# Optimization experiments

Hardware: AMD Instinct MI355X
Metric: run time of the kernel (lower is better)

Reference implementation:

```python
import jax, jax.numpy as jnp
import numpy as np

N_NODES = 150000
D = 64
N_EDGES = 2000000  # bidirectional: 2 * num_train_edges


def setup_inputs() -> dict:
    key = jax.random.key(0)
    k1, k2, k3, k4, k5 = jax.random.split(key, 5)
    nodes_emb = jax.random.normal(k1, (N_NODES, D), dtype=jnp.float32)
    src = jax.random.randint(k2, (N_EDGES,), 0, N_NODES, dtype=jnp.int64 if jax.config.jax_enable_x64 else jnp.int32).astype(jnp.int32)
    dst = jax.random.randint(k3, (N_EDGES,), 0, N_NODES, dtype=jnp.int32)
    W1 = jax.random.normal(k4, (2 * D, D), dtype=jnp.float32) * (1.0 / np.sqrt(2 * D))
    b1 = jnp.zeros((D,), dtype=jnp.float32)
    W2 = jax.random.normal(k5, (D, 1), dtype=jnp.float32) * (1.0 / np.sqrt(D))
    b2 = jnp.zeros((1,), dtype=jnp.float32)
    return {"nodes_emb": nodes_emb, "src": src, "dst": dst,
            "W1": W1, "b1": b1, "W2": W2, "b2": b2}


def reference(nodes_emb, src, dst, W1, b1, W2, b2):
    # Gather per-edge endpoint embeddings and concat: [E, 2D]
    emb_src = nodes_emb[src]          # [E, D]
    emb_dst = nodes_emb[dst]          # [E, D]
    edge_emb = jnp.concatenate([emb_src, emb_dst], axis=1)  # [E, 2D]
    # 2-layer MLP edge scorer: Linear(2D->D) -> ReLU -> Linear(D->1)
    h = jax.nn.relu(edge_emb @ W1 + b1)  # [E, D]
    edge_logits = h @ W2 + b2            # [E, 1]
    return edge_logits
```

## Files before the change

kernel.cpp:

```cpp
#include <hip/hip_runtime.h>
#include <math.h>

typedef __attribute__((ext_vector_type(8))) short bf16x8;
typedef __attribute__((ext_vector_type(4))) float f32x4;
typedef __attribute__((ext_vector_type(2))) unsigned int u32x2;
typedef __attribute__((ext_vector_type(4))) unsigned int u32x4;
typedef unsigned long long u64;

#define LDSTR 136
#define TPW 8
#define NREP 128
#define NBKT 64

static __device__ __forceinline__ unsigned int pack2bf(float x, float y) {
  unsigned int ux = __builtin_bit_cast(unsigned int, x);
  ux += 0x7fffu + ((ux >> 16) & 1u);
  unsigned int uy = __builtin_bit_cast(unsigned int, y);
  uy += 0x7fffu + ((uy >> 16) & 1u);
  return (ux >> 16) | (uy & 0xffff0000u);
}
static __device__ __forceinline__ unsigned short f2bf_s(float x) {
  unsigned int ux = __builtin_bit_cast(unsigned int, x);
  ux += 0x7fffu + ((ux >> 16) & 1u);
  return (unsigned short)(ux >> 16);
}
static __device__ __forceinline__ bf16x8 make_afrag(float4 lo, float4 hi) {
  u32x4 p;
  p[0] = pack2bf(lo.x, lo.y);
  p[1] = pack2bf(lo.z, lo.w);
  p[2] = pack2bf(hi.x, hi.y);
  p[3] = pack2bf(hi.z, hi.w);
  return __builtin_bit_cast(bf16x8, p);
}

static __device__ __forceinline__ unsigned int q8(float v, float inv) {
  return (unsigned int)((int)rintf(v * inv) + 128);
}

static __device__ __forceinline__ float dot8i(u32x2 P, u32x2 Q, float sp, float sq,
                                              const float* w2v) {
  const float t_ = -128.f * (sp + sq);
  float acc = 0.f;
  #pragma unroll
  for (int k2 = 0; k2 < 2; ++k2) {
    const unsigned int pd = P[k2], qd = Q[k2];
    #pragma unroll
    for (int b = 0; b < 4; ++b) {
      float pf = (float)((pd >> (8 * b)) & 0xffu);
      float qf = (float)((qd >> (8 * b)) & 0xffu);
      float h = __builtin_fmaf(pf, sp, __builtin_fmaf(qf, sq, t_));
      h = fmaxf(h, 0.f);
      acc = __builtin_fmaf(h, w2v[k2 * 4 + b], acc);
    }
  }
  return acc;
}

__global__ __launch_bounds__(256) void node_proj(
    const float* __restrict__ emb, const float* __restrict__ W1,
    const float* __restrict__ b1,
    unsigned int* __restrict__ P8, unsigned int* __restrict__ Q8,
    float* __restrict__ SP, float* __restrict__ SQ, int N, int ntiles)
{
  __shared__ unsigned short ls_w1t[64 * LDSTR];
  const int tid  = threadIdx.x;
  const int wave = tid >> 6;
  const int lane = tid & 63;
  const int l15  = lane & 15;
  const int quad = lane >> 4;

  for (int i = tid; i < 64 * 128; i += 256) {
    int k = i >> 6, n = i & 63;
    ls_w1t[n * LDSTR + k] = f2bf_s(W1[i]);
  }
  __syncthreads();

  float b1q[4];
  #pragma unroll
  for (int tn = 0; tn < 4; ++tn) b1q[tn] = b1[tn * 16 + l15];

  bf16x8 bfragP[4][2], bfragQ[4][2];
  #pragma unroll
  for (int tn = 0; tn < 4; ++tn)
    #pragma unroll
    for (int s = 0; s < 2; ++s) {
      bfragP[tn][s] = *(const bf16x8*)&ls_w1t[(tn * 16 + l15) * LDSTR + s * 32 + quad * 8];
      bfragQ[tn][s] = *(const bf16x8*)&ls_w1t[(tn * 16 + l15) * LDSTR + 64 + s * 32 + quad * 8];
    }

  for (int tile = blockIdx.x * 4 + wave; tile < ntiles; tile += gridDim.x * 4) {
    const int base = tile * 16;

    bf16x8 afr0, afr1;
    {
      int node = base + l15;
      node = (node < N) ? node : N - 1;
      const float* rp = emb + (long long)node * 64 + quad * 8;
      afr0 = make_afrag(*(const float4*)(rp),      *(const float4*)(rp + 4));
      afr1 = make_afrag(*(const float4*)(rp + 32), *(const float4*)(rp + 36));
    }

    f32x4 aP[4], aQ[4];
    #pragma unroll
    for (int tn = 0; tn < 4; ++tn) { aP[tn] = (f32x4){0,0,0,0}; aQ[tn] = (f32x4){0,0,0,0}; }
    #pragma unroll
    for (int tn = 0; tn < 4; ++tn) {
      aP[tn] = __builtin_amdgcn_mfma_f32_16x16x32_bf16(afr0, bfragP[tn][0], aP[tn], 0, 0, 0);
      aQ[tn] = __builtin_amdgcn_mfma_f32_16x16x32_bf16(afr0, bfragQ[tn][0], aQ[tn], 0, 0, 0);
      aP[tn] = __builtin_amdgcn_mfma_f32_16x16x32_bf16(afr1, bfragP[tn][1], aP[tn], 0, 0, 0);
      aQ[tn] = __builtin_amdgcn_mfma_f32_16x16x32_bf16(afr1, bfragQ[tn][1], aQ[tn], 0, 0, 0);
    }

    #pragma unroll
    for (int r = 0; r < 4; ++r) {
      const int m = base + quad * 4 + r;
      float vp0 = aP[0][r], vp1 = aP[1][r], vp2 = aP[2][r], vp3 = aP[3][r];
      float vq0 = aQ[0][r] + b1q[0], vq1 = aQ[1][r] + b1q[1];
      float vq2 = aQ[2][r] + b1q[2], vq3 = aQ[3][r] + b1q[3];

      float mp = fmaxf(fmaxf(fabsf(vp0), fabsf(vp1)), fmaxf(fabsf(vp2), fabsf(vp3)));
      float mq = fmaxf(fmaxf(fabsf(vq0), fabsf(vq1)), fmaxf(fabsf(vq2), fabsf(vq3)));
      mp = fmaxf(mp, __shfl_xor(mp, 1)); mq = fmaxf(mq, __shfl_xor(mq, 1));
      mp = fmaxf(mp, __shfl_xor(mp, 2)); mq = fmaxf(mq, __shfl_xor(mq, 2));
      mp = fmaxf(mp, __shfl_xor(mp, 4)); mq = fmaxf(mq, __shfl_xor(mq, 4));
      mp = fmaxf(mp, __shfl_xor(mp, 8)); mq = fmaxf(mq, __shfl_xor(mq, 8));

      const float invP = (mp > 0.f) ? 127.f / mp : 0.f;
      const float invQ = (mq > 0.f) ? 127.f / mq : 0.f;

      if (m < N) {
        unsigned int pw = q8(vp0, invP) | (q8(vp1, invP) << 8) |
                          (q8(vp2, invP) << 16) | (q8(vp3, invP) << 24);
        unsigned int qw = q8(vq0, invQ) | (q8(vq1, invQ) << 8) |
                          (q8(vq2, invQ) << 16) | (q8(vq3, invQ) << 24);
        P8[(long long)m * 16 + l15] = pw;
        Q8[(long long)m * 16 + l15] = qw;
        if (l15 == 0) {
          SP[m] = mp * (1.f / 127.f);
          SQ[m] = mq * (1.f / 127.f);
        }
      }
    }
  }
}

__global__ __launch_bounds__(256) void bucketize(
    const int* __restrict__ src, const int* __restrict__ dst,
    const float* __restrict__ SP, const float* __restrict__ SQ,
    u32x2* __restrict__ seg, unsigned short* __restrict__ posrec,
    unsigned int* __restrict__ cntT, int E, int ndiv, int cap)
{
  __shared__ unsigned int curs[NBKT];
  const int r = blockIdx.x;
  const int per = (E + NREP - 1) / NREP;
  const int lo = r * per;
  const int hi = (lo + per < E) ? lo + per : E;
  for (int i = threadIdx.x; i < NBKT; i += 256) curs[i] = 0;
  __syncthreads();

  for (int e0 = lo + threadIdx.x; e0 < hi; e0 += 1024) {
    const int e1 = e0 + 256, e2 = e0 + 512, e3 = e0 + 768;
    const int e1c = (e1 < hi) ? e1 : hi - 1;
    const int e2c = (e2 < hi) ? e2 : hi - 1;
    const int e3c = (e3 < hi) ? e3 : hi - 1;
    const int s0 = src[e0],  d0 = dst[e0];
    const int s1 = src[e1c], d1 = dst[e1c];
    const int s2 = src[e2c], d2 = dst[e2c];
    const int s3 = src[e3c], d3 = dst[e3c];
    const float sp0 = SP[s0], sq0 = SQ[d0];
    const float sp1 = SP[s1], sq1 = SQ[d1];
    const float sp2 = SP[s2], sq2 = SQ[d2];
    const float sp3 = SP[s3], sq3 = SQ[d3];

#define BK_PROC(EE, SS, DD, SPV, SQV)                                         \
    {                                                                         \
      const int bi = (SS) / ndiv, bj = (DD) / ndiv;                           \
      const int bkt = bi * 8 + bj;                                            \
      const unsigned int pos = atomicAdd(&curs[bkt], 1u);                     \
      unsigned short pr = 0xFFFFu;                                            \
      if (pos < (unsigned)cap) {                                              \
        u32x2 ev;                                                             \
        ev[0] = (unsigned)((SS) - bi * ndiv) |                                \
                ((unsigned)((DD) - bj * ndiv) << 15);                         \
        ev[1] = ((unsigned)f2bf_s(SPV) << 16) | (unsigned)f2bf_s(SQV);        \
        seg[((size_t)(r * NBKT + bkt)) * cap + pos] = ev;                     \
        pr = (unsigned short)(((unsigned)bkt << 9) | pos);                    \
      }                                                                       \
      posrec[EE] = pr;                                                        \
    }

    BK_PROC(e0, s0, d0, sp0, sq0);
    if (e1 < hi) BK_PROC(e1, s1, d1, sp1, sq1);
    if (e2 < hi) BK_PROC(e2, s2, d2, sp2, sq2);
    if (e3 < hi) BK_PROC(e3, s3, d3, sp3, sq3);
#undef BK_PROC
  }
  __syncthreads();
  for (int bkt = threadIdx.x; bkt < NBKT; bkt += 256) {
    unsigned int c = curs[bkt];
    cntT[bkt * NREP + r] = (c < (unsigned)cap) ? c : (unsigned)cap;
  }
}

__global__ __launch_bounds__(256) void edge_score_seg(
    const unsigned int* __restrict__ P8, const unsigned int* __restrict__ Q8,
    const u32x2* __restrict__ seg, const unsigned int* __restrict__ cntT,
    const float* __restrict__ W2, const float* __restrict__ b2,
    float* __restrict__ tmp, int cap, int ndiv)
{
  const int tid  = threadIdx.x;
  const int lane = tid & 63;
  const int sv   = lane & 7;
  const int g    = lane >> 3;
  const int k    = blockIdx.x & 7;
  const int tblk = blockIdx.x >> 3;
  const int wgid = tblk * 4 + (tid >> 6);
  const int r    = wgid >> 3;
  const int sub  = wgid & 7;

  float w2v[8];
  #pragma unroll
  for (int j = 0; j < 8; ++j) {
    const int pos = sv * 8 + j;
    const int ch  = (pos & 3) * 16 + (pos >> 2);
    w2v[j] = W2[ch];
  }
  const float b2v = b2[0];
  const int sd = sv * 2;
  const int sbase = k * ndiv;

  int cnts[8];
  #pragma unroll
  for (int j = 0; j < 8; ++j) cnts[j] = (int)cntT[(k * 8 + j) * NREP + r];

  #pragma unroll 1
  for (int j = 0; j < 8; ++j) {
    const int b = k * 8 + j;
    const int dbase = j * ndiv;
    const int cnt = cnts[j];
    const int chunk = (cnt + 7) >> 3;
    const int lo = sub * chunk;
    const int hi = (cnt < lo + chunk) ? cnt : lo + chunk;
    if (lo >= hi) continue;
    const u32x2* sgp = seg + (size_t)(r * NBKT + b) * cap;
    float* tp = tmp + (size_t)(r * NBKT + b) * cap;

    #pragma unroll 2
    for (int m = lo + g; m < hi; m += 8) {
      const u32x2 v = sgp[m];
      const int s_ = sbase + (int)(v[0] & 0x7FFFu);
      const int d_ = dbase + (int)(v[0] >> 15);
      const float sp = __builtin_bit_cast(float, v[1] & 0xffff0000u);
      const float sq = __builtin_bit_cast(float, v[1] << 16);

      const u32x2 pv = *(const u32x2*)(P8 + s_ * 16 + sd);
      const u32x2 qv = *(const u32x2*)(Q8 + d_ * 16 + sd);

      float acc = dot8i(pv, qv, sp, sq, w2v);
      acc += __shfl_xor(acc, 1);
      acc += __shfl_xor(acc, 2);
      acc += __shfl_xor(acc, 4);
      if (sv == 0) tp[m] = acc + b2v;
    }
  }
}

__global__ __launch_bounds__(256) void unscatter(
    const unsigned short* __restrict__ posrec, const float* __restrict__ tmp,
    float* __restrict__ out,
    const int* __restrict__ src, const int* __restrict__ dst,
    const unsigned int* __restrict__ P8, const unsigned int* __restrict__ Q8,
    const float* __restrict__ SP, const float* __restrict__ SQ,
    const float* __restrict__ W2, const float* __restrict__ b2,
    int E, int per, int cap)
{
  const int r   = blockIdx.x >> 3;
  const int sub = blockIdx.x & 7;
  const int lo_r = r * per;
  int lenr = E - lo_r;
  if (lenr <= 0) return;
  if (lenr > per) lenr = per;
  const int chunk = (lenr + 7) >> 3;
  const int lo = lo_r + sub * chunk;
  int hi = lo + chunk;
  const int end_r = lo_r + lenr;
  if (hi > end_r) hi = end_r;
  const float* tb = tmp + (size_t)r * NBKT * cap;

  for (int e = lo + threadIdx.x; e < hi; e += 256) {
    const unsigned int pr = posrec[e];
    if (pr != 0xFFFFu) {
      out[e] = tb[(pr >> 9) * cap + (pr & 511u)];
    } else {
      const int s_ = src[e], d_ = dst[e];
      const float sp = SP[s_], sq = SQ[d_];
      const float t_ = -128.f * (sp + sq);
      float acc = 0.f;
      for (int w = 0; w < 16; ++w) {
        const unsigned int pd = P8[(size_t)s_ * 16 + w];
        const unsigned int qd = Q8[(size_t)d_ * 16 + w];
        for (int bb = 0; bb < 4; ++bb) {
          const int pos = w * 4 + bb;
          const int ch  = (pos & 3) * 16 + (pos >> 2);
          float pf = (float)((pd >> (8 * bb)) & 0xffu);
          float qf = (float)((qd >> (8 * bb)) & 0xffu);
          float h = __builtin_fmaf(pf, sp, __builtin_fmaf(qf, sq, t_));
          h = fmaxf(h, 0.f);
          acc = __builtin_fmaf(h, W2[ch], acc);
        }
      }
      out[e] = acc + b2[0];
    }
  }
}

__global__ __launch_bounds__(256) void edge_score(
    const unsigned int* __restrict__ P8, const unsigned int* __restrict__ Q8,
    const float* __restrict__ SP, const float* __restrict__ SQ,
    const int* __restrict__ src, const int* __restrict__ dst,
    const float* __restrict__ W2, const float* __restrict__ b2,
    float* __restrict__ out, int E)
{
  const int tid  = blockIdx.x * 256 + threadIdx.x;
  const int lane = threadIdx.x & 63;
  const int s    = lane & 7;
  const int g    = lane >> 3;
  const int wid  = tid >> 6;
  const int step = gridDim.x * 4 * 32;

  float w2v[8];
  #pragma unroll
  for (int j = 0; j < 8; ++j) {
    const int pos = s * 8 + j;
    const int ch  = (pos & 3) * 16 + (pos >> 2);
    w2v[j] = W2[ch];
  }
  const float b2v = b2[0];
  const int sd = s * 2;

  int e0 = wid * 32;
  if (e0 >= E) return;

  int iA, iB, iC, iD, jA, jB, jC, jD;
  {
    const int eA = e0 + g,      eAc = (eA < E) ? eA : E - 1;
    const int eB = e0 + 8 + g,  eBc = (eB < E) ? eB : E - 1;
    const int eC = e0 + 16 + g, eCc = (eC < E) ? eC : E - 1;
    const int eD = e0 + 24 + g, eDc = (eD < E) ? eD : E - 1;
    iA = src[eAc]; jA = dst[eAc];
    iB = src[eBc]; jB = dst[eBc];
    iC = src[eCc]; jC = dst[eCc];
    iD = src[eDc]; jD = dst[eDc];
  }
  float spA = SP[iA], sqA = SQ[jA];
  float spB = SP[iB], sqB = SQ[jB];
  float spC = SP[iC], sqC = SQ[jC];
  float spD = SP[iD], sqD = SQ[jD];

  while (true) {
    const u32x2 pA = *(const u32x2*)(P8 + iA * 16 + sd);
    const u32x2 qA = *(const u32x2*)(Q8 + jA * 16 + sd);
    const u32x2 pB = *(const u32x2*)(P8 + iB * 16 + sd);
    const u32x2 qB = *(const u32x2*)(Q8 + jB * 16 + sd);
    const u32x2 pC = *(const u32x2*)(P8 + iC * 16 + sd);
    const u32x2 qC = *(const u32x2*)(Q8 + jC * 16 + sd);
    const u32x2 pD = *(const u32x2*)(P8 + iD * 16 + sd);
    const u32x2 qD = *(const u32x2*)(Q8 + jD * 16 + sd);

    const int en = e0 + step;
    const bool more = (en < E);
    int nA = iA, nB = iB, nC = iC, nD = iD;
    int mA = jA, mB = jB, mC = jC, mD = jD;
    if (more) {
      const int fA = en + g,      fAc = (fA < E) ? fA : E - 1;
      const int fB = en + 8 + g,  fBc = (fB < E) ? fB : E - 1;
      const int fC = en + 16 + g, fCc = (fC < E) ? fC : E - 1;
      const int fD = en + 24 + g, fDc = (fD < E) ? fD : E - 1;
      nA = src[fAc]; mA = dst[fAc];
      nB = src[fBc]; mB = dst[fBc];
      nC = src[fCc]; mC = dst[fCc];
      nD = src[fDc]; mD = dst[fDc];
    }

    float accA = dot8i(pA, qA, spA, sqA, w2v);
    float accB = dot8i(pB, qB, spB, sqB, w2v);
    float accC = dot8i(pC, qC, spC, sqC, w2v);
    float accD = dot8i(pD, qD, spD, sqD, w2v);

    accA += __shfl_xor(accA, 1); accB += __shfl_xor(accB, 1);
    accC += __shfl_xor(accC, 1); accD += __shfl_xor(accD, 1);
    accA += __shfl_xor(accA, 2); accB += __shfl_xor(accB, 2);
    accC += __shfl_xor(accC, 2); accD += __shfl_xor(accD, 2);
    accA += __shfl_xor(accA, 4); accB += __shfl_xor(accB, 4);
    accC += __shfl_xor(accC, 4); accD += __shfl_xor(accD, 4);

    if (s == 0) {
      const int eA = e0 + g;
      const int eB = e0 + 8 + g;
      const int eC = e0 + 16 + g;
      const int eD = e0 + 24 + g;
      if (eA < E) out[eA] = accA + b2v;
      if (eB < E) out[eB] = accB + b2v;
      if (eC < E) out[eC] = accC + b2v;
      if (eD < E) out[eD] = accD + b2v;
    }

    if (!more) break;
    iA = nA; iB = nB; iC = nC; iD = nD;
    jA = mA; jB = mB; jC = mC; jD = mD;
    spA = SP[iA]; sqA = SQ[jA];
    spB = SP[iB]; sqB = SQ[jB];
    spC = SP[iC]; sqC = SQ[jC];
    spD = SP[iD]; sqD = SQ[jD];
    e0 = en;
  }
}

__global__ __launch_bounds__(256) void edge_mlp_f32(
    const float* __restrict__ nodes_emb, const int* __restrict__ src,
    const int* __restrict__ dst, const float* __restrict__ W1,
    const float* __restrict__ b1, const float* __restrict__ W2,
    const float* __restrict__ b2, float* __restrict__ out, int E)
{
  __shared__ unsigned short ls_w1t[64 * LDSTR];
  __shared__ float ls_b1[64];
  __shared__ float ls_w2[64];
  const int tid = threadIdx.x, wave = tid >> 6, lane = tid & 63;
  const int l15 = lane & 15, quad = lane >> 4;
  for (int i = tid; i < 64 * 128; i += 256) {
    int n = i >> 7, k = i & 127;
    ls_w1t[n * LDSTR + k] = f2bf_s(W1[k * 64 + n]);
  }
  if (tid < 64) { ls_b1[tid] = b1[tid]; ls_w2[tid] = W2[tid]; }
  __syncthreads();
  bf16x8 bfrag[4][4];
  #pragma unroll
  for (int tn = 0; tn < 4; ++tn)
    #pragma unroll
    for (int s = 0; s < 4; ++s)
      bfrag[tn][s] = *(const bf16x8*)&ls_w1t[(tn * 16 + l15) * LDSTR + s * 32 + quad * 8];
  float myb1[4], myw2[4];
  #pragma unroll
  for (int tn = 0; tn < 4; ++tn) { myb1[tn] = ls_b1[tn*16+l15]; myw2[tn] = ls_w2[tn*16+l15]; }
  const float b2v = b2[0];
  const int wave_base = blockIdx.x * (TPW * 64) + wave * (TPW * 16);
  #pragma unroll 1
  for (int t = 0; t < TPW; ++t) {
    const int tile_base = wave_base + t * 16;
    if (tile_base >= E) break;
    const int e = tile_base + l15;
    const int si = src[e], di = dst[e];
    const float* srow = nodes_emb + (long long)si * 64 + quad * 8;
    const float* drow = nodes_emb + (long long)di * 64 + quad * 8;
    float4 v0 = *(const float4*)(srow),      v1 = *(const float4*)(srow + 4);
    float4 v2 = *(const float4*)(srow + 32), v3 = *(const float4*)(srow + 36);
    float4 v4 = *(const float4*)(drow),      v5 = *(const float4*)(drow + 4);
    float4 v6 = *(const float4*)(drow + 32), v7 = *(const float4*)(drow + 36);
    bf16x8 afr[4] = {make_afrag(v0,v1), make_afrag(v2,v3), make_afrag(v4,v5), make_afrag(v6,v7)};
    f32x4 acc[4];
    #pragma unroll
    for (int tn = 0; tn < 4; ++tn) acc[tn] = (f32x4){0.f,0.f,0.f,0.f};
    #pragma unroll
    for (int s = 0; s < 4; ++s)
      #pragma unroll
      for (int tn = 0; tn < 4; ++tn)
        acc[tn] = __builtin_amdgcn_mfma_f32_16x16x32_bf16(afr[s], bfrag[tn][s], acc[tn], 0, 0, 0);
    #pragma unroll
    for (int r = 0; r < 4; ++r) {
      float p = 0.f;
      #pragma unroll
      for (int tn = 0; tn < 4; ++tn) {
        float h = fmaxf(acc[tn][r] + myb1[tn], 0.f);
        p = __builtin_fmaf(h, myw2[tn], p);
      }
      p += __shfl_xor(p, 1); p += __shfl_xor(p, 2);
      p += __shfl_xor(p, 4); p += __shfl_xor(p, 8);
      if (l15 == 0) out[tile_base + quad * 4 + r] = p + b2v;
    }
  }
}

extern "C" void kernel_launch(void* const* d_in, const int* in_sizes, int n_in,
                              void* d_out, int out_size, void* d_ws, size_t ws_size,
                              hipStream_t stream) {
  const float* nodes_emb = (const float*)d_in[0];
  const int*   src       = (const int*)d_in[1];
  const int*   dst       = (const int*)d_in[2];
  const float* W1        = (const float*)d_in[3];
  const float* b1        = (const float*)d_in[4];
  const float* W2        = (const float*)d_in[5];
  const float* b2        = (const float*)d_in[6];
  float* out = (float*)d_out;

  const int E = in_sizes[1];
  const int nodes_elems = in_sizes[0];
  const int N = nodes_elems / 64;
  const int ntiles = (N + 15) / 16;
  const int ndiv = (N + 7) / 8;
  const int per  = (E + NREP - 1) / NREP;

  const long long cells = (long long)NBKT * NREP;
  const int perCell = (int)((E + cells - 1) / cells);
  const int sig = (int)ceilf(sqrtf((float)(perCell > 0 ? perCell : 1)));
  const int cap = perCell + 5 * sig + 8;

  const size_t szRow   = (size_t)N * 64;
  const size_t offSP   = szRow * 2;
  const size_t offSQ   = offSP + (size_t)N * 4;
  const size_t offCnt  = offSQ + (size_t)N * 4;
  const size_t offPos  = offCnt + (size_t)NBKT * NREP * 4;
  const size_t offSeg  = (offPos + (size_t)E * 2 + 7) & ~(size_t)7;
  const size_t offTmp  = offSeg + (size_t)NBKT * NREP * (size_t)cap * 8;
  const size_t need_full = offTmp + (size_t)NBKT * NREP * (size_t)cap * 4;
  const size_t need_mid  = offCnt;

  if (ws_size >= need_mid && N > 0) {
    unsigned int* P8 = (unsigned int*)d_ws;
    unsigned int* Q8 = (unsigned int*)((char*)d_ws + szRow);
    float* SP = (float*)((char*)d_ws + offSP);
    float* SQ = (float*)((char*)d_ws + offSQ);
    hipLaunchKernelGGL(node_proj, dim3(512), dim3(256), 0, stream,
                       nodes_emb, W1, b1, P8, Q8, SP, SQ, N, ntiles);
    if (ws_size >= need_full && cap <= 511 && ndiv <= 32767) {
      unsigned int*   cntT   = (unsigned int*)((char*)d_ws + offCnt);
      unsigned short* posrec = (unsigned short*)((char*)d_ws + offPos);
      u32x2*          seg    = (u32x2*)((char*)d_ws + offSeg);
      float*          tmp    = (float*)((char*)d_ws + offTmp);
      hipLaunchKernelGGL(bucketize, dim3(NREP), dim3(256), 0, stream,
                         src, dst, SP, SQ, seg, posrec, cntT, E, ndiv, cap);
      hipLaunchKernelGGL(edge_score_seg, dim3(2048), dim3(256), 0, stream,
                         P8, Q8, seg, cntT, W2, b2, tmp, cap, ndiv);
      hipLaunchKernelGGL(unscatter, dim3(NREP * 8), dim3(256), 0, stream,
                         posrec, tmp, out, src, dst, P8, Q8, SP, SQ, W2, b2,
                         E, per, cap);
    } else {
      hipLaunchKernelGGL(edge_score, dim3(4096), dim3(256), 0, stream,
                         P8, Q8, SP, SQ, src, dst, W2, b2, out, E);
    }
  } else {
    const int epb = TPW * 64;
    const int blocks = (E + epb - 1) / epb;
    hipLaunchKernelGGL(edge_mlp_f32, dim3(blocks), dim3(256), 0, stream,
                       nodes_emb, src, dst, W1, b1, W2, b2, out, E);
  }
}
```

Measured before the change: 206.9 us.

## Split bucketize across 8 blocks per replica using global atomic counters

The bucketize kernel now launches eight blocks per replica instead of one, and each block handles one eighth of the replica's edge range. Because the per-bucket cursors are now shared across blocks, they move from LDS to global-memory atomics on cntT, which is zeroed by a memset before the launch. The clamping to cap moves into the consumer kernel. This raises the low grid occupancy of 128 blocks, but pays for it with global atomic contention, an extra memset, and nondeterministic slot order within buckets.

```diff
diff --git a/kernel.cpp b/kernel.cpp
--- a/kernel.cpp
+++ b/kernel.cpp
@@ -150,19 +150,25 @@
     u32x2* __restrict__ seg, unsigned short* __restrict__ posrec,
     unsigned int* __restrict__ cntT, int E, int ndiv, int cap)
 {
-  __shared__ unsigned int curs[NBKT];
-  const int r = blockIdx.x;
+  const int r   = blockIdx.x >> 3;
+  const int sub = blockIdx.x & 7;
   const int per = (E + NREP - 1) / NREP;
-  const int lo = r * per;
-  const int hi = (lo + per < E) ? lo + per : E;
-  for (int i = threadIdx.x; i < NBKT; i += 256) curs[i] = 0;
-  __syncthreads();
-
-  for (int e0 = lo + threadIdx.x; e0 < hi; e0 += 1024) {
+  const int lo_r = r * per;
+  int len = E - lo_r;
+  if (len <= 0) return;
+  if (len > per) len = per;
+  const int chunk = (len + 7) >> 3;
+  const int slo = lo_r + sub * chunk;
+  int shi = slo + chunk;
+  const int end_r = lo_r + len;
+  if (shi > end_r) shi = end_r;
+  if (slo >= shi) return;
+
+  for (int e0 = slo + threadIdx.x; e0 < shi; e0 += 1024) {
     const int e1 = e0 + 256, e2 = e0 + 512, e3 = e0 + 768;
-    const int e1c = (e1 < hi) ? e1 : hi - 1;
-    const int e2c = (e2 < hi) ? e2 : hi - 1;
-    const int e3c = (e3 < hi) ? e3 : hi - 1;
+    const int e1c = (e1 < shi) ? e1 : shi - 1;
+    const int e2c = (e2 < shi) ? e2 : shi - 1;
+    const int e3c = (e3 < shi) ? e3 : shi - 1;
     const int s0 = src[e0],  d0 = dst[e0];
     const int s1 = src[e1c], d1 = dst[e1c];
     const int s2 = src[e2c], d2 = dst[e2c];
@@ -176,7 +182,7 @@
     {                                                                         \
       const int bi = (SS) / ndiv, bj = (DD) / ndiv;                           \
       const int bkt = bi * 8 + bj;                                            \
-      const unsigned int pos = atomicAdd(&curs[bkt], 1u);                     \
+      const unsigned int pos = atomicAdd(&cntT[bkt * NREP + r], 1u);          \
       unsigned short pr = 0xFFFFu;                                            \
       if (pos < (unsigned)cap) {                                              \
         u32x2 ev;                                                             \
@@ -190,15 +196,10 @@
     }
 
     BK_PROC(e0, s0, d0, sp0, sq0);
-    if (e1 < hi) BK_PROC(e1, s1, d1, sp1, sq1);
-    if (e2 < hi) BK_PROC(e2, s2, d2, sp2, sq2);
-    if (e3 < hi) BK_PROC(e3, s3, d3, sp3, sq3);
+    if (e1 < shi) BK_PROC(e1, s1, d1, sp1, sq1);
+    if (e2 < shi) BK_PROC(e2, s2, d2, sp2, sq2);
+    if (e3 < shi) BK_PROC(e3, s3, d3, sp3, sq3);
 #undef BK_PROC
-  }
-  __syncthreads();
-  for (int bkt = threadIdx.x; bkt < NBKT; bkt += 256) {
-    unsigned int c = curs[bkt];
-    cntT[bkt * NREP + r] = (c < (unsigned)cap) ? c : (unsigned)cap;
   }
 }
 
@@ -231,7 +232,10 @@
 
   int cnts[8];
   #pragma unroll
-  for (int j = 0; j < 8; ++j) cnts[j] = (int)cntT[(k * 8 + j) * NREP + r];
+  for (int j = 0; j < 8; ++j) {
+    int c = (int)cntT[(k * 8 + j) * NREP + r];
+    cnts[j] = (c < cap) ? c : cap;
+  }
 
   #pragma unroll 1
   for (int j = 0; j < 8; ++j) {
@@ -526,7 +530,8 @@
       unsigned short* posrec = (unsigned short*)((char*)d_ws + offPos);
       u32x2*          seg    = (u32x2*)((char*)d_ws + offSeg);
       float*          tmp    = (float*)((char*)d_ws + offTmp);
-      hipLaunchKernelGGL(bucketize, dim3(NREP), dim3(256), 0, stream,
+      hipMemsetAsync(cntT, 0, (size_t)NBKT * NREP * 4, stream);
+      hipLaunchKernelGGL(bucketize, dim3(NREP * 8), dim3(256), 0, stream,
                          src, dst, SP, SQ, seg, posrec, cntT, E, ndiv, cap);
       hipLaunchKernelGGL(edge_score_seg, dim3(2048), dim3(256), 0, stream,
                          P8, Q8, seg, cntT, W2, b2, tmp, cap, ndiv);
```

After: 298.6 us. +44.3%, slower.
